# Performance work log

Measured on AMD Instinct MI355X. Metric: run time of the kernel, lower is better.

Reference implementation:

```python
import jax, jax.numpy as jnp
import numpy as np

NUM_CODES = 8192
EMBED_DIM = 256
N_TOKENS = 65536
COMMITMENT_COST = 0.25


def setup_inputs() -> dict:
    key = jax.random.key(0)
    k1, k2 = jax.random.split(key)
    inputs = jax.random.normal(k1, (N_TOKENS, EMBED_DIM), dtype=jnp.float32)
    # torch init: uniform(-1/num_codes, 1/num_codes); use normal-scale equivalent via uniform
    weight = jax.random.uniform(k2, (NUM_CODES, EMBED_DIM), dtype=jnp.float32,
                                minval=-1.0 / NUM_CODES, maxval=1.0 / NUM_CODES)
    return {"inputs": inputs, "weight": weight}


def reference(inputs, weight):
    inputs_sq = jnp.sum(inputs * inputs, axis=1, keepdims=True)      # (N, 1)
    embed_sq = jnp.sum(weight * weight, axis=1)                      # (K,)
    distances = inputs_sq + embed_sq - 2.0 * (inputs @ weight.T)     # (N, K)
    indices = jnp.argmin(distances, axis=1)                          # (N,)
    quantized = jnp.take(weight, indices, axis=0)                    # (N, D)

    codebook_loss = jnp.mean((quantized - jax.lax.stop_gradient(inputs)) ** 2)
    commit_loss = jnp.mean((inputs - jax.lax.stop_gradient(quantized)) ** 2)
    vq_loss = codebook_loss + COMMITMENT_COST * commit_loss

    # straight-through estimator
    quantized_st = inputs + jax.lax.stop_gradient(quantized - inputs)
    return quantized_st, indices, vq_loss, codebook_loss, commit_loss
```

## Files before the change

### kernel.cpp

```cpp
#include <hip/hip_runtime.h>

#define N_TOK  65536
#define N_CODE 8192
#define DIM    256

typedef _Float16 f16;
typedef _Float16 f16x8 __attribute__((ext_vector_type(8)));
typedef float    f32x4 __attribute__((ext_vector_type(4)));

__global__ __launch_bounds__(256) void rowsq_kernel(const float* __restrict__ src,
                                                    float* __restrict__ dst, int nrows) {
    int row  = blockIdx.x * 4 + (threadIdx.x >> 6);
    int lane = threadIdx.x & 63;
    if (row >= nrows) return;
    float4 v = ((const float4*)(src + (size_t)row * DIM))[lane];
    float s = v.x * v.x + v.y * v.y + v.z * v.z + v.w * v.w;
#pragma unroll
    for (int off = 32; off; off >>= 1) s += __shfl_down(s, off, 64);
    if (lane == 0) dst[row] = s;
}

__global__ __launch_bounds__(256) void splitw_kernel(const float* __restrict__ W,
                                                     f16* __restrict__ W1,
                                                     f16* __restrict__ W2) {
    int f = blockIdx.x * 256 + threadIdx.x;
    float4 v = ((const float4*)W)[f];
    union { f16 h[4]; uint2 u; } p1, p2;
    float e[4] = {v.x, v.y, v.z, v.w};
#pragma unroll
    for (int i = 0; i < 4; ++i) {
        float ws = e[i] * 16384.0f;
        f16 w1 = (f16)ws;
        float r = (ws - (float)w1) * 2048.0f;
        p1.h[i] = w1; p2.h[i] = (f16)r;
    }
    ((uint2*)W1)[f] = p1.u;
    ((uint2*)W2)[f] = p2.u;
}

__global__ __launch_bounds__(512, 2) void argmin_mfma2(
    const float* __restrict__ X, const f16* __restrict__ W1, const f16* __restrict__ W2,
    const float* __restrict__ sxq, const float* __restrict__ esq,
    int* __restrict__ out_idx) {

    __shared__ char wbuf[65536];

    const int tid  = threadIdx.x;
    const int lane = tid & 63;
    const int wv   = tid >> 6;
    const int cl   = lane & 15;
    const int q    = lane >> 4;
    const int wavetok0 = blockIdx.x * 256 + wv * 32;

    f16x8 a1[2][8], a2[2][8];
#pragma unroll
    for (int mt = 0; mt < 2; ++mt)
#pragma unroll
        for (int s = 0; s < 8; ++s) {
            const float* p = X + (size_t)(wavetok0 + mt * 16 + cl) * DIM + s * 32 + q * 8;
            float4 v0 = ((const float4*)p)[0];
            float4 v1 = ((const float4*)p)[1];
            float e[8] = {v0.x, v0.y, v0.z, v0.w, v1.x, v1.y, v1.z, v1.w};
#pragma unroll
            for (int j = 0; j < 8; ++j) {
                f16 h = (f16)e[j];
                float r = (e[j] - (float)h) * 2048.0f;
                a1[mt][s][j] = h;
                a2[mt][s][j] = (f16)r;
            }
        }

    float sxr[8];
#pragma unroll
    for (int mt = 0; mt < 2; ++mt)
#pragma unroll
        for (int r = 0; r < 4; ++r)
            sxr[mt * 4 + r] = sxq[wavetok0 + mt * 16 + q * 4 + r];

    float bestd[8];
    int   besti[8];
#pragma unroll
    for (int i = 0; i < 8; ++i) { bestd[i] = 3.4e38f; besti[i] = 0x7fffffff; }

    auto stage = [&](int ct2, int sel) {
#pragma unroll
        for (int t = 0; t < 4; ++t) {
            int fi = wv * 4 + t;
            int L  = fi >> 4;
            int cp = fi & 15;
            int c  = 2 * cp + (lane >> 5);
            int o  = (lane & 31) ^ (c & 7);
            const f16* gsrc = (L ? W2 : W1) + (size_t)(ct2 * 32 + c) * DIM + o * 8;
            char* ldst = wbuf + sel * 32768 + L * 16384 + cp * 1024;
            __builtin_amdgcn_global_load_lds(
                (const __attribute__((address_space(1))) unsigned int*)gsrc,
                (__attribute__((address_space(3))) unsigned int*)ldst, 16, 0, 0);
        }
    };

    stage(0, 0);
    __syncthreads();

    for (int ct = 0; ct < N_CODE / 32; ++ct) {
        if (ct + 1 < N_CODE / 32) stage(ct + 1, (ct + 1) & 1);

        float se0 = esq[ct * 32 + cl];
        float se1 = esq[ct * 32 + 16 + cl];

        f32x4 mainA[2][2], cA[2][2], cB[2][2];
#pragma unroll
        for (int mt = 0; mt < 2; ++mt)
#pragma unroll
            for (int nt = 0; nt < 2; ++nt) {
                mainA[mt][nt] = (f32x4){0.f, 0.f, 0.f, 0.f};
                cA[mt][nt]    = (f32x4){0.f, 0.f, 0.f, 0.f};
                cB[mt][nt]    = (f32x4){0.f, 0.f, 0.f, 0.f};
            }

        const char* base = wbuf + (ct & 1) * 32768;
#pragma unroll
        for (int s = 0; s < 8; ++s) {
            f16x8 b1[2], b2[2];
#pragma unroll
            for (int nt = 0; nt < 2; ++nt) {
                int off = ((nt * 16 + cl) * 32 + (((s * 4 + q) ^ (cl & 7)))) * 16;
                b1[nt] = *(const f16x8*)(base + off);
                b2[nt] = *(const f16x8*)(base + 16384 + off);
            }
#pragma unroll
            for (int mt = 0; mt < 2; ++mt)
#pragma unroll
                for (int nt = 0; nt < 2; ++nt) {
                    mainA[mt][nt] = __builtin_amdgcn_mfma_f32_16x16x32_f16(a1[mt][s], b1[nt], mainA[mt][nt], 0, 0, 0);
                    cA[mt][nt]    = __builtin_amdgcn_mfma_f32_16x16x32_f16(a1[mt][s], b2[nt], cA[mt][nt], 0, 0, 0);
                    cB[mt][nt]    = __builtin_amdgcn_mfma_f32_16x16x32_f16(a2[mt][s], b1[nt], cB[mt][nt], 0, 0, 0);
                }
        }

#pragma unroll
        for (int mt = 0; mt < 2; ++mt)
#pragma unroll
            for (int nt = 0; nt < 2; ++nt)
#pragma unroll
                for (int r = 0; r < 4; ++r) {
                    float cr = cA[mt][nt][r] + cB[mt][nt][r];
                    float mc = fmaf(cr, 4.8828125e-4f, mainA[mt][nt][r]);
                    float t1 = sxr[mt * 4 + r] + (nt ? se1 : se0);
                    float d  = fmaf(-1.220703125e-4f, mc, t1);
                    int slot = mt * 4 + r;
                    if (d < bestd[slot]) {
                        bestd[slot] = d;
                        besti[slot] = ct * 32 + nt * 16 + cl;
                    }
                }
        __syncthreads();
    }

#pragma unroll
    for (int slot = 0; slot < 8; ++slot) {
        float d = bestd[slot];
        int   i = besti[slot];
#pragma unroll
        for (int off = 1; off < 16; off <<= 1) {
            float od = __shfl_xor(d, off, 64);
            int   oi = __shfl_xor(i, off, 64);
            if (od < d || (od == d && oi < i)) { d = od; i = oi; }
        }
        if (cl == 0)
            out_idx[wavetok0 + (slot >> 2) * 16 + q * 4 + (slot & 3)] = i;
    }
}

__global__ __launch_bounds__(256) void finalize_kernel(
    const float* __restrict__ X, const float* __restrict__ W,
    const int* __restrict__ idx, float* __restrict__ outQ,
    float* __restrict__ outI, double* __restrict__ accum) {
    __shared__ double wsum[4];
    int wid  = threadIdx.x >> 6;
    int lane = threadIdx.x & 63;
    int token = blockIdx.x * 4 + wid;
    int id = idx[token];
    float4 x = ((const float4*)(X + (size_t)token * DIM))[lane];
    float4 qv = ((const float4*)(W + (size_t)id * DIM))[lane];
    float4 o;
    o.x = x.x + (qv.x - x.x);
    o.y = x.y + (qv.y - x.y);
    o.z = x.z + (qv.z - x.z);
    o.w = x.w + (qv.w - x.w);
    ((float4*)(outQ + (size_t)token * DIM))[lane] = o;
    float dx = x.x - qv.x, dy = x.y - qv.y, dz = x.z - qv.z, dw = x.w - qv.w;
    float s = dx * dx + dy * dy + dz * dz + dw * dw;
#pragma unroll
    for (int off = 32; off; off >>= 1) s += __shfl_down(s, off, 64);
    if (lane == 0) {
        outI[token] = (float)id;
        wsum[wid] = (double)s;
    }
    __syncthreads();
    if (threadIdx.x == 0) {
        double t = wsum[0] + wsum[1] + wsum[2] + wsum[3];
        atomicAdd(accum, t);
    }
}

__global__ void scalars_kernel(const double* __restrict__ accum, float* __restrict__ out) {
    double mse = *accum / (double)((size_t)N_TOK * DIM);
    float c = (float)mse;
    out[0] = c + 0.25f * c;
    out[1] = c;
    out[2] = c;
}

extern "C" void kernel_launch(void* const* d_in, const int* in_sizes, int n_in,
                              void* d_out, int out_size, void* d_ws, size_t ws_size,
                              hipStream_t stream) {
    const float* X = (const float*)d_in[0];
    const float* W = (const float*)d_in[1];

    float* outQ = (float*)d_out;
    float* outI = outQ + (size_t)N_TOK * DIM;
    float* outS = outI + N_TOK;

    char* ws = (char*)d_ws;
    double* accum = (double*)ws;
    float* esq = (float*)(ws + 64);
    float* sxq = (float*)(ws + 64 + 32768);
    int*   idx = (int*)(ws + 64 + 32768 + 262144);
    f16*   W1  = (f16*)(ws + (1 << 20));
    f16*   W2  = (f16*)(ws + (1 << 20) + 4194304);

    hipMemsetAsync(accum, 0, sizeof(double), stream);
    splitw_kernel<<<N_CODE * DIM / 4 / 256, 256, 0, stream>>>(W, W1, W2);
    rowsq_kernel<<<N_CODE / 4, 256, 0, stream>>>(W, esq, N_CODE);
    rowsq_kernel<<<N_TOK / 4, 256, 0, stream>>>(X, sxq, N_TOK);
    argmin_mfma2<<<N_TOK / 256, 512, 0, stream>>>(X, W1, W2, sxq, esq, idx);
    finalize_kernel<<<N_TOK / 4, 256, 0, stream>>>(X, W, idx, outQ, outI, accum);
    scalars_kernel<<<1, 1, 0, stream>>>(accum, outS);
}
```

Before: 930.2 us.

## Widen code tile to 64, prefetch LDS fragments, merge cross-term accumulators

Each pipeline stage now loads 64 codes instead of 32 into a doubled 128 KB LDS double buffer, which halves the number of loop iterations and block barriers. Inside each 32-code half, the B fragments for the next k-slice are loaded from LDS into registers before the current slice's MFMAs run, so LDS reads overlap with matrix math. The two correction-term accumulators are folded into one, which saves registers and a per-element add. The larger LDS footprint allows only one block per CU, but the grid has 256 blocks, so this likely makes little difference on a 256-CU part.

```diff
diff --git a/kernel.cpp b/kernel.cpp
--- a/kernel.cpp
+++ b/kernel.cpp
@@ -38,18 +38,19 @@
     ((uint2*)W2)[f] = p2.u;
 }
 
-__global__ __launch_bounds__(512, 2) void argmin_mfma2(
+__global__ __launch_bounds__(512, 2) void argmin_mfma3(
     const float* __restrict__ X, const f16* __restrict__ W1, const f16* __restrict__ W2,
     const float* __restrict__ sxq, const float* __restrict__ esq,
     int* __restrict__ out_idx) {
 
-    __shared__ char wbuf[65536];
+    __shared__ char wbuf[131072];
 
     const int tid  = threadIdx.x;
     const int lane = tid & 63;
     const int wv   = tid >> 6;
     const int cl   = lane & 15;
     const int q    = lane >> 4;
+    const int cl7  = cl & 7;
     const int wavetok0 = blockIdx.x * 256 + wv * 32;
 
     f16x8 a1[2][8], a2[2][8];
@@ -84,14 +85,14 @@
 
     auto stage = [&](int ct2, int sel) {
 #pragma unroll
-        for (int t = 0; t < 4; ++t) {
-            int fi = wv * 4 + t;
-            int L  = fi >> 4;
-            int cp = fi & 15;
+        for (int t = 0; t < 8; ++t) {
+            int fi = wv * 8 + t;
+            int L  = fi >> 5;
+            int cp = fi & 31;
             int c  = 2 * cp + (lane >> 5);
             int o  = (lane & 31) ^ (c & 7);
-            const f16* gsrc = (L ? W2 : W1) + (size_t)(ct2 * 32 + c) * DIM + o * 8;
-            char* ldst = wbuf + sel * 32768 + L * 16384 + cp * 1024;
+            const f16* gsrc = (L ? W2 : W1) + (size_t)(ct2 * 64 + c) * DIM + o * 8;
+            char* ldst = wbuf + sel * 65536 + L * 32768 + cp * 1024;
             __builtin_amdgcn_global_load_lds(
                 (const __attribute__((address_space(1))) unsigned int*)gsrc,
                 (__attribute__((address_space(3))) unsigned int*)ldst, 16, 0, 0);
@@ -101,58 +102,71 @@
     stage(0, 0);
     __syncthreads();
 
-    for (int ct = 0; ct < N_CODE / 32; ++ct) {
-        if (ct + 1 < N_CODE / 32) stage(ct + 1, (ct + 1) & 1);
-
-        float se0 = esq[ct * 32 + cl];
-        float se1 = esq[ct * 32 + 16 + cl];
-
-        f32x4 mainA[2][2], cA[2][2], cB[2][2];
-#pragma unroll
-        for (int mt = 0; mt < 2; ++mt)
-#pragma unroll
-            for (int nt = 0; nt < 2; ++nt) {
-                mainA[mt][nt] = (f32x4){0.f, 0.f, 0.f, 0.f};
-                cA[mt][nt]    = (f32x4){0.f, 0.f, 0.f, 0.f};
-                cB[mt][nt]    = (f32x4){0.f, 0.f, 0.f, 0.f};
-            }
-
-        const char* base = wbuf + (ct & 1) * 32768;
-#pragma unroll
-        for (int s = 0; s < 8; ++s) {
-            f16x8 b1[2], b2[2];
-#pragma unroll
-            for (int nt = 0; nt < 2; ++nt) {
-                int off = ((nt * 16 + cl) * 32 + (((s * 4 + q) ^ (cl & 7)))) * 16;
-                b1[nt] = *(const f16x8*)(base + off);
-                b2[nt] = *(const f16x8*)(base + 16384 + off);
-            }
-#pragma unroll
-            for (int mt = 0; mt < 2; ++mt)
-#pragma unroll
-                for (int nt = 0; nt < 2; ++nt) {
-                    mainA[mt][nt] = __builtin_amdgcn_mfma_f32_16x16x32_f16(a1[mt][s], b1[nt], mainA[mt][nt], 0, 0, 0);
-                    cA[mt][nt]    = __builtin_amdgcn_mfma_f32_16x16x32_f16(a1[mt][s], b2[nt], cA[mt][nt], 0, 0, 0);
-                    cB[mt][nt]    = __builtin_amdgcn_mfma_f32_16x16x32_f16(a2[mt][s], b1[nt], cB[mt][nt], 0, 0, 0);
-                }
-        }
-
-#pragma unroll
-        for (int mt = 0; mt < 2; ++mt)
-#pragma unroll
-            for (int nt = 0; nt < 2; ++nt)
-#pragma unroll
-                for (int r = 0; r < 4; ++r) {
-                    float cr = cA[mt][nt][r] + cB[mt][nt][r];
-                    float mc = fmaf(cr, 4.8828125e-4f, mainA[mt][nt][r]);
-                    float t1 = sxr[mt * 4 + r] + (nt ? se1 : se0);
-                    float d  = fmaf(-1.220703125e-4f, mc, t1);
-                    int slot = mt * 4 + r;
-                    if (d < bestd[slot]) {
-                        bestd[slot] = d;
-                        besti[slot] = ct * 32 + nt * 16 + cl;
+    for (int ct = 0; ct < N_CODE / 64; ++ct) {
+        if (ct + 1 < N_CODE / 64) stage(ct + 1, (ct + 1) & 1);
+        const char* base = wbuf + (ct & 1) * 65536;
+
+#pragma unroll
+        for (int h = 0; h < 2; ++h) {
+            float se0 = esq[ct * 64 + h * 32 + cl];
+            float se1 = esq[ct * 64 + h * 32 + 16 + cl];
+
+            f32x4 mainA[4], crossA[4];
+#pragma unroll
+            for (int t = 0; t < 4; ++t) {
+                mainA[t]  = (f32x4){0.f, 0.f, 0.f, 0.f};
+                crossA[t] = (f32x4){0.f, 0.f, 0.f, 0.f};
+            }
+
+            f16x8 fb1[2][2], fb2[2][2];
+#pragma unroll
+            for (int nt2 = 0; nt2 < 2; ++nt2) {
+                int n   = h * 32 + nt2 * 16 + cl;
+                int off = n * 512 + (((0 * 4 + q) ^ cl7) * 16);
+                fb1[0][nt2] = *(const f16x8*)(base + off);
+                fb2[0][nt2] = *(const f16x8*)(base + 32768 + off);
+            }
+#pragma unroll
+            for (int s = 0; s < 8; ++s) {
+                int cur = s & 1;
+                if (s < 7) {
+                    int nx = cur ^ 1;
+#pragma unroll
+                    for (int nt2 = 0; nt2 < 2; ++nt2) {
+                        int n   = h * 32 + nt2 * 16 + cl;
+                        int off = n * 512 + ((((s + 1) * 4 + q) ^ cl7) * 16);
+                        fb1[nx][nt2] = *(const f16x8*)(base + off);
+                        fb2[nx][nt2] = *(const f16x8*)(base + 32768 + off);
                     }
                 }
+#pragma unroll
+                for (int mt = 0; mt < 2; ++mt)
+#pragma unroll
+                    for (int nt2 = 0; nt2 < 2; ++nt2) {
+                        int t = mt * 2 + nt2;
+                        mainA[t]  = __builtin_amdgcn_mfma_f32_16x16x32_f16(a1[mt][s], fb1[cur][nt2], mainA[t], 0, 0, 0);
+                        crossA[t] = __builtin_amdgcn_mfma_f32_16x16x32_f16(a2[mt][s], fb1[cur][nt2], crossA[t], 0, 0, 0);
+                        crossA[t] = __builtin_amdgcn_mfma_f32_16x16x32_f16(a1[mt][s], fb2[cur][nt2], crossA[t], 0, 0, 0);
+                    }
+            }
+
+#pragma unroll
+            for (int mt = 0; mt < 2; ++mt)
+#pragma unroll
+                for (int nt2 = 0; nt2 < 2; ++nt2)
+#pragma unroll
+                    for (int r = 0; r < 4; ++r) {
+                        int t = mt * 2 + nt2;
+                        float mc = fmaf(crossA[t][r], 4.8828125e-4f, mainA[t][r]);
+                        float t1 = sxr[mt * 4 + r] + (nt2 ? se1 : se0);
+                        float d  = fmaf(-1.220703125e-4f, mc, t1);
+                        int slot = mt * 4 + r;
+                        if (d < bestd[slot]) {
+                            bestd[slot] = d;
+                            besti[slot] = ct * 64 + h * 32 + nt2 * 16 + cl;
+                        }
+                    }
+        }
         __syncthreads();
     }
 
@@ -233,7 +247,7 @@
     splitw_kernel<<<N_CODE * DIM / 4 / 256, 256, 0, stream>>>(W, W1, W2);
     rowsq_kernel<<<N_CODE / 4, 256, 0, stream>>>(W, esq, N_CODE);
     rowsq_kernel<<<N_TOK / 4, 256, 0, stream>>>(X, sxq, N_TOK);
-    argmin_mfma2<<<N_TOK / 256, 512, 0, stream>>>(X, W1, W2, sxq, esq, idx);
+    argmin_mfma3<<<N_TOK / 256, 512, 0, stream>>>(X, W1, W2, sxq, esq, idx);
     finalize_kernel<<<N_TOK / 4, 256, 0, stream>>>(X, W, idx, outQ, outI, accum);
     scalars_kernel<<<1, 1, 0, stream>>>(accum, outS);
 }
```

New measurement: 987.5 us. +6.2%, slower.
